# Kernel tuning notes

Measured on AMD Instinct MI355X. Metric: run time of the kernel, lower is better.

Reference implementation:

```python
import jax, jax.numpy as jnp
import numpy as np

V_TH = 1.0
LENS, SCALE, HIGHT, GAMMA = 0.5, 6.0, 0.15, 0.5  # MultiGaussian surrogate constants (DH-SNN)


def _gauss(x, mu, sigma):
    return jnp.exp(-((x - mu) ** 2) / (2.0 * sigma ** 2)) / (jnp.sqrt(2.0 * jnp.pi) * sigma)


@jax.custom_vjp
def spike_fn(x):
    return (x > 0).astype(x.dtype)


def _spike_fwd(x):
    return spike_fn(x), x


def _spike_bwd(x, g):
    sg = GAMMA * (_gauss(x, 0.0, LENS) * (1.0 + HIGHT)
                  - _gauss(x, LENS, SCALE * LENS) * HIGHT
                  - _gauss(x, -LENS, SCALE * LENS) * HIGHT)
    return (g * sg,)


spike_fn.defvjp(_spike_fwd, _spike_bwd)


def setup_inputs() -> dict:
    key = jax.random.key(0)
    ks = jax.random.split(key, 12)
    B, T, I, H, O = 128, 784, 512, 512, 10
    xavier_in = lambda k, sh: jax.random.normal(k, sh, jnp.float32) * jnp.sqrt(2.0 / (sh[0] + sh[1]))
    return {
        'input_data': jax.random.normal(ks[0], (B, T, I), jnp.float32),
        'W1': xavier_in(ks[1], (H, I)),
        'b1': jnp.zeros((H,), jnp.float32),
        'W2': xavier_in(ks[2], (H, I)),
        'b2': jnp.zeros((H,), jnp.float32),
        'tau_m': jax.random.uniform(ks[3], (H,), jnp.float32, 0.0, 4.0),
        'tau_n1': jax.random.uniform(ks[4], (H,), jnp.float32, 2.0, 6.0),
        'tau_n2': jax.random.uniform(ks[5], (H,), jnp.float32, -4.0, 0.0),
        'Wr': xavier_in(ks[6], (O, H)),
        'br': jnp.zeros((O,), jnp.float32),
        'mem0': jax.random.uniform(ks[7], (B, H), jnp.float32),
        'spike0': jax.random.uniform(ks[8], (B, H), jnp.float32),
    }


def reference(input_data, W1, b1, W2, b2, tau_m, tau_n1, tau_n2, Wr, br, mem0, spike0):
    # Batched branch projections for all timesteps (big GEMMs, done once)
    d1_all = jnp.einsum('bti,hi->bth', input_data, W1) + b1  # [B,T,H]
    d2_all = jnp.einsum('bti,hi->bth', input_data, W2) + b2

    alpha = jax.nn.sigmoid(tau_m)    # membrane decay
    beta1 = jax.nn.sigmoid(tau_n1)   # branch-1 dendritic decay
    beta2 = jax.nn.sigmoid(tau_n2)   # branch-2 dendritic decay

    B, H = mem0.shape
    d1_init = jnp.zeros((B, H), input_data.dtype)
    d2_init = jnp.zeros((B, H), input_data.dtype)

    def step(carry, xs):
        mem, spk, d1, d2 = carry
        d1_t, d2_t = xs
        d1 = beta1 * d1 + (1.0 - beta1) * d1_t
        d2 = beta2 * d2 + (1.0 - beta2) * d2_t
        total = d1 + d2
        mem = mem * alpha + (1.0 - alpha) * total - V_TH * spk
        spk = spike_fn(mem - V_TH)
        return (mem, spk, d1, d2), spk

    xs = (jnp.swapaxes(d1_all, 0, 1), jnp.swapaxes(d2_all, 0, 1))  # [T,B,H]
    _, spikes = jax.lax.scan(step, (mem0, spike0, d1_init, d2_init), xs)
    spikes = jnp.swapaxes(spikes, 0, 1)  # [B,T,H]
    out = jnp.einsum('bth,oh->bto', spikes, Wr) + br  # readout per timestep
    return out
```

## Files before the change

kernel.cpp:

```cpp
#include <hip/hip_runtime.h>
#include <cmath>

#define HD 512
#define IN 512
#define TT 784
#define BB 128
#define MH 50176

typedef short short8 __attribute__((ext_vector_type(8)));
typedef unsigned short ushort8 __attribute__((ext_vector_type(8)));
typedef float floatx4 __attribute__((ext_vector_type(4)));

#define GLDS(gp, lp) __builtin_amdgcn_global_load_lds( \
    (const __attribute__((address_space(1))) void*)(gp), \
    (__attribute__((address_space(3))) void*)(lp), 16, 0, 0)

__device__ __forceinline__ unsigned short bf16_rne(float x) {
    unsigned u = __float_as_uint(x);
    unsigned r = u + 0x7FFFu + ((u >> 16) & 1u);
    return (unsigned short)(r >> 16);
}
__device__ __forceinline__ float bf16_f(unsigned short s) {
    return __uint_as_float(((unsigned)s) << 16);
}

__global__ __launch_bounds__(256) void split3(
    const float* __restrict__ src, unsigned short* __restrict__ p1,
    unsigned short* __restrict__ p2, unsigned short* __restrict__ p3, long n8)
{
    long g = (long)blockIdx.x * 256 + threadIdx.x;
    if (g >= n8) return;
    const float* xp = src + g * 8;
    ushort8 o1, o2, o3;
#pragma unroll
    for (int j = 0; j < 8; ++j) {
        float x = xp[j];
        unsigned short s1 = bf16_rne(x);
        float r1 = x - bf16_f(s1);
        unsigned short s2 = bf16_rne(r1);
        float r2 = r1 - bf16_f(s2);
        unsigned short s3 = bf16_rne(r2);
        o1[j] = s1; o2[j] = s2; o3[j] = s3;
    }
    *(ushort8*)(p1 + g * 8) = o1;
    *(ushort8*)(p2 + g * 8) = o2;
    *(ushort8*)(p3 + g * 8) = o3;
}

__global__ __launch_bounds__(256, 2) void gemm_bf16x3(
    const unsigned short* __restrict__ Xp,
    const unsigned short* __restrict__ Wp,
    const float* __restrict__ b1, const float* __restrict__ b2,
    float* __restrict__ d1buf, float* __restrict__ d2buf)
{
    __shared__ unsigned short lds[6][128][32];
    unsigned short* lflat = &lds[0][0][0];
    const int tid  = threadIdx.x;
    const int lane = tid & 63;
    const int w    = tid >> 6;
    const int wg = (blockIdx.x & 7) * 392 + (blockIdx.x >> 3);
    const int pm = wg >> 3;
    const int pn = wg & 7;
    const int m0 = pm * 128;
    const int n0 = pn * 128;

    const unsigned short* gp[12];
    {
        const int rsub = lane >> 2;
        const int csub = (lane & 3) * 8;
#pragma unroll
        for (int j = 0; j < 12; ++j) {
            int seg = w * 12 + j;
            int p = seg >> 3, sub = seg & 7;
            int row16 = sub * 16 + rsub;
            gp[j] = (p < 3)
              ? Xp + ((size_t)p * MH + m0 + row16) * IN + csub
              : Wp + ((size_t)(p - 3) * 1024 + n0 + row16) * IN + csub;
        }
    }

    floatx4 acc[4][4];
#pragma unroll
    for (int i = 0; i < 4; ++i)
#pragma unroll
        for (int j = 0; j < 4; ++j) acc[i][j] = (floatx4){0.f, 0.f, 0.f, 0.f};

    const int wm = w >> 1, wn = w & 1;
    const int c16 = lane & 15;
    const int q8  = (lane >> 4) * 8;

    for (int ks = 0; ks < IN; ks += 32) {
#pragma unroll
        for (int j = 0; j < 12; ++j)
            GLDS(gp[j] + ks, lflat + (size_t)(w * 12 + j) * 512);
        __syncthreads();

        short8 Bf[3][4];
#pragma unroll
        for (int p = 0; p < 3; ++p)
#pragma unroll
            for (int fj = 0; fj < 4; ++fj)
                Bf[p][fj] = *(const short8*)&lds[3 + p][wn * 64 + fj * 16 + c16][q8];

#pragma unroll
        for (int fi = 0; fi < 4; ++fi) {
            const int r = wm * 64 + fi * 16 + c16;
            short8 a1 = *(const short8*)&lds[0][r][q8];
            short8 a2 = *(const short8*)&lds[1][r][q8];
            short8 a3 = *(const short8*)&lds[2][r][q8];
#pragma unroll
            for (int fj = 0; fj < 4; ++fj) {
                floatx4 c = acc[fi][fj];
                c = __builtin_amdgcn_mfma_f32_16x16x32_bf16(a3, Bf[0][fj], c, 0, 0, 0);
                c = __builtin_amdgcn_mfma_f32_16x16x32_bf16(a2, Bf[1][fj], c, 0, 0, 0);
                c = __builtin_amdgcn_mfma_f32_16x16x32_bf16(a1, Bf[2][fj], c, 0, 0, 0);
                c = __builtin_amdgcn_mfma_f32_16x16x32_bf16(a2, Bf[0][fj], c, 0, 0, 0);
                c = __builtin_amdgcn_mfma_f32_16x16x32_bf16(a1, Bf[1][fj], c, 0, 0, 0);
                c = __builtin_amdgcn_mfma_f32_16x16x32_bf16(a1, Bf[0][fj], c, 0, 0, 0);
                acc[fi][fj] = c;
            }
        }
        __syncthreads();
    }

    const int quad = lane >> 4;
    const bool first = (n0 < HD);
    const float* bias = first ? b1 : b2;
    float* obuf = first ? d1buf : d2buf;
    const int nb = n0 & (HD - 1);
    float bv[4];
#pragma unroll
    for (int fj = 0; fj < 4; ++fj) bv[fj] = bias[nb + wn * 64 + fj * 16 + c16];
#pragma unroll
    for (int fi = 0; fi < 4; ++fi) {
#pragma unroll
        for (int fj = 0; fj < 4; ++fj) {
            int n = nb + wn * 64 + fj * 16 + c16;
#pragma unroll
            for (int r = 0; r < 4; ++r) {
                int m = m0 + wm * 64 + fi * 16 + quad * 4 + r;
                obuf[(size_t)m * HD + n] = acc[fi][fj][r] + bv[fj];
            }
        }
    }
}

#define LOADG(g, A1, A2) do {                                        \
    _Pragma("unroll")                                                \
    for (int i = 0; i < 16; ++i) {                                   \
        A1[i] = p1[(size_t)((g) * 16 + i) * HD];                     \
        A2[i] = p2[(size_t)((g) * 16 + i) * HD];                     \
    } } while (0)

#define COMPG(g, A1, A2) do {                                        \
    unsigned int wq = 0;                                             \
    _Pragma("unroll")                                                \
    for (int i = 0; i < 16; ++i) {                                   \
        d1 = be1 * d1 + (1.f - be1) * A1[i];                         \
        d2 = be2 * d2 + (1.f - be2) * A2[i];                         \
        float tot = d1 + d2;                                         \
        mem = mem * alpha + (1.f - alpha) * tot - spk;               \
        bool fire = (mem - 1.0f) > 0.f;                              \
        spk = fire ? 1.f : 0.f;                                      \
        wq |= (fire ? 1u : 0u) << i;                                 \
    }                                                                \
    sp[(size_t)(g) * HD] = (unsigned short)wq; } while (0)

__global__ __launch_bounds__(64) void scan_half(
    const float* __restrict__ d1buf, const float* __restrict__ d2buf,
    const float* __restrict__ tau_m, const float* __restrict__ tau_n1,
    const float* __restrict__ tau_n2,
    const float* __restrict__ mem0, const float* __restrict__ spike0,
    unsigned short* __restrict__ spikes, int b0)
{
    const int gid = blockIdx.x * 64 + threadIdx.x;
    const int h  = gid & (HD - 1);
    const int bl = gid >> 9;
    const int b  = b0 + bl;
    const float alpha = 1.f / (1.f + expf(-tau_m[h]));
    const float be1   = 1.f / (1.f + expf(-tau_n1[h]));
    const float be2   = 1.f / (1.f + expf(-tau_n2[h]));
    float mem = mem0[b * HD + h];
    float spk = spike0[b * HD + h];
    float d1 = 0.f, d2 = 0.f;
    const float* p1 = d1buf + (size_t)bl * TT * HD + h;
    const float* p2 = d2buf + (size_t)bl * TT * HD + h;
    unsigned short* sp = spikes + (size_t)b * (TT / 16) * HD + h;

    float a1A[16], a2A[16], a1B[16], a2B[16];
    LOADG(0, a1A, a2A);
#pragma unroll 1
    for (int g = 0; g < 48; g += 2) {
        LOADG(g + 1, a1B, a2B);
        COMPG(g,     a1A, a2A);
        LOADG(g + 2, a1A, a2A);
        COMPG(g + 1, a1B, a2B);
    }
    COMPG(48, a1A, a2A);
}

__global__ __launch_bounds__(256) void readout(
    const unsigned short* __restrict__ spikes,
    const float* __restrict__ Wr, const float* __restrict__ br,
    float* __restrict__ out)
{
    __shared__ float WrS[10 * HD];
    __shared__ float brS[10];
    const int tid = threadIdx.x;
    for (int i = tid; i < 10 * HD; i += 256) WrS[i] = Wr[i];
    if (tid < 10) brS[tid] = br[tid];
    __syncthreads();

    const int gid = blockIdx.x * 256 + tid;
    const int t = gid % TT;
    const int b = gid / TT;
    const int tw  = t >> 4;
    const int bit = t & 15;
    const unsigned short* row = spikes + ((size_t)b * (TT / 16) + tw) * HD;

    float acc[10];
#pragma unroll
    for (int o = 0; o < 10; ++o) acc[o] = brS[o];

    for (int h = 0; h < HD; ++h) {
        float s = (float)((row[h] >> bit) & 1);
#pragma unroll
        for (int o = 0; o < 10; ++o) acc[o] = fmaf(s, WrS[o * HD + h], acc[o]);
    }
    float* op = out + (size_t)gid * 10;
#pragma unroll
    for (int o = 0; o < 10; ++o) op[o] = acc[o];
}

extern "C" void kernel_launch(void* const* d_in, const int* in_sizes, int n_in,
                              void* d_out, int out_size, void* d_ws, size_t ws_size,
                              hipStream_t stream)
{
    const float* X      = (const float*)d_in[0];
    const float* W1     = (const float*)d_in[1];
    const float* b1     = (const float*)d_in[2];
    const float* W2     = (const float*)d_in[3];
    const float* b2     = (const float*)d_in[4];
    const float* tau_m  = (const float*)d_in[5];
    const float* tau_n1 = (const float*)d_in[6];
    const float* tau_n2 = (const float*)d_in[7];
    const float* Wr     = (const float*)d_in[8];
    const float* br     = (const float*)d_in[9];
    const float* mem0   = (const float*)d_in[10];
    const float* spike0 = (const float*)d_in[11];
    float* out = (float*)d_out;

    char* p = (char*)d_ws;
    unsigned short* Wp = (unsigned short*)p;  p += (size_t)3 * 1024 * IN * 2;
    unsigned short* Xp = (unsigned short*)p;  p += (size_t)3 * MH * IN * 2;
    float* d1buf = (float*)p;                 p += (size_t)MH * HD * 4;
    float* d2buf = (float*)p;                 p += (size_t)MH * HD * 4;
    unsigned short* spikes = (unsigned short*)p;

    const size_t WPS = (size_t)1024 * IN;
    const size_t XPS = (size_t)MH * IN;

    split3<<<dim3(128), dim3(256), 0, stream>>>(
        W1, Wp, Wp + WPS, Wp + 2 * WPS, (long)HD * IN / 8);
    split3<<<dim3(128), dim3(256), 0, stream>>>(
        W2, Wp + (size_t)HD * IN, Wp + WPS + (size_t)HD * IN,
        Wp + 2 * WPS + (size_t)HD * IN, (long)HD * IN / 8);

    for (int half = 0; half < 2; ++half) {
        split3<<<dim3((unsigned)(((long)MH * IN / 8 + 255) / 256)), dim3(256), 0, stream>>>(
            X + (size_t)half * MH * IN, Xp, Xp + XPS, Xp + 2 * XPS, (long)MH * IN / 8);
        gemm_bf16x3<<<dim3(392 * 8), dim3(256), 0, stream>>>(
            Xp, Wp, b1, b2, d1buf, d2buf);
        scan_half<<<dim3(512), dim3(64), 0, stream>>>(
            d1buf, d2buf, tau_m, tau_n1, tau_n2, mem0, spike0,
            spikes, half * 64);
    }
    readout<<<dim3(BB * TT / 256), dim3(256), 0, stream>>>(spikes, Wr, br, out);
}
```

Measured before the change: 1.096 ms.

## Triple-buffer GEMM K loop with 32x32 MFMA and swizzled LDS layout

Rewrites the bf16x3 GEMM main loop to use a three-stage LDS ring with global_load_lds prefetch and explicit vmcnt waits, so global loads overlap with MFMA work instead of being serialized by barriers. The K step shrinks to 16 and the compute switches from 16x16x32 to 32x32x16 MFMA tiles, with an XOR-swizzled LDS layout meant to avoid bank conflicts. LDS rises to 72KB dynamic, which may limit occupancy to two blocks per CU, and the hand-written waitcnt logic is fragile.

Result: slower. 1.219 ms (+11.2%).

```diff
diff --git a/kernel.cpp b/kernel.cpp
--- a/kernel.cpp
+++ b/kernel.cpp
@@ -10,6 +10,7 @@
 typedef short short8 __attribute__((ext_vector_type(8)));
 typedef unsigned short ushort8 __attribute__((ext_vector_type(8)));
 typedef float floatx4 __attribute__((ext_vector_type(4)));
+typedef float floatx16 __attribute__((ext_vector_type(16)));
 
 #define GLDS(gp, lp) __builtin_amdgcn_global_load_lds( \
     (const __attribute__((address_space(1))) void*)(gp), \
@@ -47,14 +48,13 @@
     *(ushort8*)(p3 + g * 8) = o3;
 }
 
-__global__ __launch_bounds__(256, 2) void gemm_bf16x3(
+__global__ __launch_bounds__(256, 2) void gemm_bf16x3_p2(
     const unsigned short* __restrict__ Xp,
     const unsigned short* __restrict__ Wp,
     const float* __restrict__ b1, const float* __restrict__ b2,
     float* __restrict__ d1buf, float* __restrict__ d2buf)
 {
-    __shared__ unsigned short lds[6][128][32];
-    unsigned short* lflat = &lds[0][0][0];
+    extern __shared__ unsigned short lds[];
     const int tid  = threadIdx.x;
     const int lane = tid & 63;
     const int w    = tid >> 6;
@@ -64,82 +64,106 @@
     const int m0 = pm * 128;
     const int n0 = pn * 128;
 
-    const unsigned short* gp[12];
+    const unsigned short* gp[6];
+    unsigned loff[6];
     {
-        const int rsub = lane >> 2;
-        const int csub = (lane & 3) * 8;
-#pragma unroll
-        for (int j = 0; j < 12; ++j) {
-            int seg = w * 12 + j;
-            int p = seg >> 3, sub = seg & 7;
-            int row16 = sub * 16 + rsub;
+        const int rsub = lane >> 1;
+        const int csub = (((lane & 1) ^ ((lane >> 3) & 1)) * 8);
+#pragma unroll
+        for (int j = 0; j < 6; ++j) {
+            int s = w * 6 + j;
+            int p = s >> 2, rb = s & 3;
             gp[j] = (p < 3)
-              ? Xp + ((size_t)p * MH + m0 + row16) * IN + csub
-              : Wp + ((size_t)(p - 3) * 1024 + n0 + row16) * IN + csub;
+              ? Xp + ((size_t)p * MH + m0 + rb * 32 + rsub) * IN + csub
+              : Wp + ((size_t)(p - 3) * 1024 + n0 + rb * 32 + rsub) * IN + csub;
+            loff[j] = (unsigned)s * 512;
         }
     }
 
-    floatx4 acc[4][4];
-#pragma unroll
-    for (int i = 0; i < 4; ++i)
-#pragma unroll
-        for (int j = 0; j < 4; ++j) acc[i][j] = (floatx4){0.f, 0.f, 0.f, 0.f};
+    floatx16 acc[2][2];
+#pragma unroll
+    for (int i = 0; i < 2; ++i)
+#pragma unroll
+        for (int j = 0; j < 2; ++j)
+#pragma unroll
+            for (int r = 0; r < 16; ++r) acc[i][j][r] = 0.f;
 
     const int wm = w >> 1, wn = w & 1;
-    const int c16 = lane & 15;
-    const int q8  = (lane >> 4) * 8;
-
-    for (int ks = 0; ks < IN; ks += 32) {
-#pragma unroll
-        for (int j = 0; j < 12; ++j)
-            GLDS(gp[j] + ks, lflat + (size_t)(w * 12 + j) * 512);
-        __syncthreads();
-
-        short8 Bf[3][4];
-#pragma unroll
-        for (int p = 0; p < 3; ++p)
-#pragma unroll
-            for (int fj = 0; fj < 4; ++fj)
-                Bf[p][fj] = *(const short8*)&lds[3 + p][wn * 64 + fj * 16 + c16][q8];
-
-#pragma unroll
-        for (int fi = 0; fi < 4; ++fi) {
-            const int r = wm * 64 + fi * 16 + c16;
-            short8 a1 = *(const short8*)&lds[0][r][q8];
-            short8 a2 = *(const short8*)&lds[1][r][q8];
-            short8 a3 = *(const short8*)&lds[2][r][q8];
-#pragma unroll
-            for (int fj = 0; fj < 4; ++fj) {
-                floatx4 c = acc[fi][fj];
-                c = __builtin_amdgcn_mfma_f32_16x16x32_bf16(a3, Bf[0][fj], c, 0, 0, 0);
-                c = __builtin_amdgcn_mfma_f32_16x16x32_bf16(a2, Bf[1][fj], c, 0, 0, 0);
-                c = __builtin_amdgcn_mfma_f32_16x16x32_bf16(a1, Bf[2][fj], c, 0, 0, 0);
-                c = __builtin_amdgcn_mfma_f32_16x16x32_bf16(a2, Bf[0][fj], c, 0, 0, 0);
-                c = __builtin_amdgcn_mfma_f32_16x16x32_bf16(a1, Bf[1][fj], c, 0, 0, 0);
-                c = __builtin_amdgcn_mfma_f32_16x16x32_bf16(a1, Bf[0][fj], c, 0, 0, 0);
-                acc[fi][fj] = c;
+    const int l31 = lane & 31;
+    const int sl8 = (((lane >> 5) ^ ((lane >> 2) & 1)) & 1) * 8;
+
+    auto compute = [&](const unsigned short* buf) {
+        short8 A[2][3], B[2][3];
+#pragma unroll
+        for (int tt = 0; tt < 2; ++tt)
+#pragma unroll
+            for (int p = 0; p < 3; ++p) {
+                A[tt][p] = *(const short8*)&buf[p * 2048 +
+                    (wm * 64 + tt * 32 + l31) * 16 + sl8];
+                B[tt][p] = *(const short8*)&buf[(3 + p) * 2048 +
+                    (wn * 64 + tt * 32 + l31) * 16 + sl8];
             }
-        }
-        __syncthreads();
-    }
-
-    const int quad = lane >> 4;
+        __builtin_amdgcn_s_setprio(1);
+#pragma unroll
+        for (int ti = 0; ti < 2; ++ti)
+#pragma unroll
+            for (int tj = 0; tj < 2; ++tj) {
+                floatx16 c = acc[ti][tj];
+                c = __builtin_amdgcn_mfma_f32_32x32x16_bf16(A[ti][2], B[tj][0], c, 0, 0, 0);
+                c = __builtin_amdgcn_mfma_f32_32x32x16_bf16(A[ti][1], B[tj][1], c, 0, 0, 0);
+                c = __builtin_amdgcn_mfma_f32_32x32x16_bf16(A[ti][0], B[tj][2], c, 0, 0, 0);
+                c = __builtin_amdgcn_mfma_f32_32x32x16_bf16(A[ti][1], B[tj][0], c, 0, 0, 0);
+                c = __builtin_amdgcn_mfma_f32_32x32x16_bf16(A[ti][0], B[tj][1], c, 0, 0, 0);
+                c = __builtin_amdgcn_mfma_f32_32x32x16_bf16(A[ti][0], B[tj][0], c, 0, 0, 0);
+                acc[ti][tj] = c;
+            }
+        __builtin_amdgcn_s_setprio(0);
+    };
+
+#define STAGE(bb, t) do {                                            \
+    _Pragma("unroll")                                                \
+    for (int j = 0; j < 6; ++j)                                      \
+        GLDS(gp[j] + (t) * 16, lds + (bb) + loff[j]);                \
+    } while (0)
+
+    STAGE(0,     0);
+    STAGE(12288, 1);
+    STAGE(24576, 2);
+
+#pragma unroll 1
+    for (int t = 0; t < 32; ++t) {
+        const int b = t - (t / 3) * 3;
+        const int bb = b * 12288;
+        if (t < 30)       asm volatile("s_waitcnt vmcnt(12)" ::: "memory");
+        else if (t == 30) asm volatile("s_waitcnt vmcnt(6)"  ::: "memory");
+        else              asm volatile("s_waitcnt vmcnt(0)"  ::: "memory");
+        __builtin_amdgcn_s_barrier();
+        __builtin_amdgcn_sched_barrier(0);
+        compute(lds + bb);
+        __builtin_amdgcn_sched_barrier(0);
+        __builtin_amdgcn_s_barrier();
+        __builtin_amdgcn_sched_barrier(0);
+        if (t < 29) STAGE(bb, t + 3);
+    }
+#undef STAGE
+
+    const int rhi = (lane >> 5) * 4;
     const bool first = (n0 < HD);
     const float* bias = first ? b1 : b2;
     float* obuf = first ? d1buf : d2buf;
     const int nb = n0 & (HD - 1);
-    float bv[4];
-#pragma unroll
-    for (int fj = 0; fj < 4; ++fj) bv[fj] = bias[nb + wn * 64 + fj * 16 + c16];
-#pragma unroll
-    for (int fi = 0; fi < 4; ++fi) {
-#pragma unroll
-        for (int fj = 0; fj < 4; ++fj) {
-            int n = nb + wn * 64 + fj * 16 + c16;
-#pragma unroll
-            for (int r = 0; r < 4; ++r) {
-                int m = m0 + wm * 64 + fi * 16 + quad * 4 + r;
-                obuf[(size_t)m * HD + n] = acc[fi][fj][r] + bv[fj];
+    float bv[2];
+#pragma unroll
+    for (int tj = 0; tj < 2; ++tj) bv[tj] = bias[nb + wn * 64 + tj * 32 + l31];
+#pragma unroll
+    for (int ti = 0; ti < 2; ++ti) {
+#pragma unroll
+        for (int tj = 0; tj < 2; ++tj) {
+            int n = nb + wn * 64 + tj * 32 + l31;
+#pragma unroll
+            for (int r = 0; r < 16; ++r) {
+                int m = m0 + wm * 64 + ti * 32 + (r & 3) + 8 * (r >> 2) + rhi;
+                obuf[(size_t)m * HD + n] = acc[ti][tj][r] + bv[tj];
             }
         }
     }
@@ -250,6 +274,14 @@
     const float* spike0 = (const float*)d_in[11];
     float* out = (float*)d_out;
 
+    static int s_attr = 0;
+    if (!s_attr) {
+        (void)hipFuncSetAttribute(
+            reinterpret_cast<const void*>(gemm_bf16x3_p2),
+            hipFuncAttributeMaxDynamicSharedMemorySize, 73728);
+        s_attr = 1;
+    }
+
     char* p = (char*)d_ws;
     unsigned short* Wp = (unsigned short*)p;  p += (size_t)3 * 1024 * IN * 2;
     unsigned short* Xp = (unsigned short*)p;  p += (size_t)3 * MH * IN * 2;
@@ -269,7 +301,7 @@
     for (int half = 0; half < 2; ++half) {
         split3<<<dim3((unsigned)(((long)MH * IN / 8 + 255) / 256)), dim3(256), 0, stream>>>(
             X + (size_t)half * MH * IN, Xp, Xp + XPS, Xp + 2 * XPS, (long)MH * IN / 8);
-        gemm_bf16x3<<<dim3(392 * 8), dim3(256), 0, stream>>>(
+        gemm_bf16x3_p2<<<dim3(392 * 8), dim3(256), 73728, stream>>>(
             Xp, Wp, b1, b2, d1buf, d2buf);
         scan_half<<<dim3(512), dim3(64), 0, stream>>>(
             d1buf, d2buf, tau_m, tau_n1, tau_n2, mem0, spike0,
```

## Fuse fp32-to-bf16x3 split of input into GEMM A-tile loading

Applied to the files above, without the earlier changes.

Removes the separate split3 pass over the large input activation tensor. The GEMM now loads fp32 X directly into registers, splits it into three bf16 parts with packed convert instructions, and writes them to LDS. The loop is software-pipelined: register prefetch of the next A tile overlaps the current compute, with explicit waitcnt and barriers. This saves a full write and re-read of the tripled bf16 copy of X, but each GEMM block now re-splits its A tile once per N-tile (8 times across the grid) and reads fp32 data, which doubles the bytes per element loaded.

Measured after the change: 937.8 us. -14.5%, faster.

```diff
diff --git a/kernel.cpp b/kernel.cpp
--- a/kernel.cpp
+++ b/kernel.cpp
@@ -10,10 +10,13 @@
 typedef short short8 __attribute__((ext_vector_type(8)));
 typedef unsigned short ushort8 __attribute__((ext_vector_type(8)));
 typedef float floatx4 __attribute__((ext_vector_type(4)));
+typedef unsigned int uintx4 __attribute__((ext_vector_type(4)));
 
 #define GLDS(gp, lp) __builtin_amdgcn_global_load_lds( \
     (const __attribute__((address_space(1))) void*)(gp), \
     (__attribute__((address_space(3))) void*)(lp), 16, 0, 0)
+
+#define CVTPK(d, a, b) asm("v_cvt_pk_bf16_f32 %0, %1, %2" : "=v"(d) : "v"(a), "v"(b))
 
 __device__ __forceinline__ unsigned short bf16_rne(float x) {
     unsigned u = __float_as_uint(x);
@@ -47,8 +50,8 @@
     *(ushort8*)(p3 + g * 8) = o3;
 }
 
-__global__ __launch_bounds__(256, 2) void gemm_bf16x3(
-    const unsigned short* __restrict__ Xp,
+__global__ __launch_bounds__(256, 2) void gemm_fused(
+    const float* __restrict__ Xf,
     const unsigned short* __restrict__ Wp,
     const float* __restrict__ b1, const float* __restrict__ b2,
     float* __restrict__ d1buf, float* __restrict__ d2buf)
@@ -64,20 +67,24 @@
     const int m0 = pm * 128;
     const int n0 = pn * 128;
 
-    const unsigned short* gp[12];
+    const unsigned short* gpb[6];
+    unsigned lofb[6];
     {
         const int rsub = lane >> 2;
         const int csub = (lane & 3) * 8;
 #pragma unroll
-        for (int j = 0; j < 12; ++j) {
-            int seg = w * 12 + j;
-            int p = seg >> 3, sub = seg & 7;
-            int row16 = sub * 16 + rsub;
-            gp[j] = (p < 3)
-              ? Xp + ((size_t)p * MH + m0 + row16) * IN + csub
-              : Wp + ((size_t)(p - 3) * 1024 + n0 + row16) * IN + csub;
+        for (int j = 0; j < 6; ++j) {
+            int s = w * 6 + j;
+            int p = s >> 3, sub = s & 7;
+            gpb[j] = Wp + ((size_t)p * 1024 + n0 + sub * 16 + rsub) * IN + csub;
+            lofb[j] = 12288u + (unsigned)s * 512;
         }
     }
+
+    const int arow  = tid >> 1;
+    const int ahalf = tid & 1;
+    const float* ga = Xf + (size_t)(m0 + arow) * IN + ahalf * 16;
+    const int awbase = arow * 32 + ahalf * 16;
 
     floatx4 acc[4][4];
 #pragma unroll
@@ -89,39 +96,94 @@
     const int c16 = lane & 15;
     const int q8  = (lane >> 4) * 8;
 
-    for (int ks = 0; ks < IN; ks += 32) {
-#pragma unroll
-        for (int j = 0; j < 12; ++j)
-            GLDS(gp[j] + ks, lflat + (size_t)(w * 12 + j) * 512);
-        __syncthreads();
-
-        short8 Bf[3][4];
-#pragma unroll
-        for (int p = 0; p < 3; ++p)
-#pragma unroll
-            for (int fj = 0; fj < 4; ++fj)
-                Bf[p][fj] = *(const short8*)&lds[3 + p][wn * 64 + fj * 16 + c16][q8];
-
-#pragma unroll
-        for (int fi = 0; fi < 4; ++fi) {
-            const int r = wm * 64 + fi * 16 + c16;
-            short8 a1 = *(const short8*)&lds[0][r][q8];
-            short8 a2 = *(const short8*)&lds[1][r][q8];
-            short8 a3 = *(const short8*)&lds[2][r][q8];
-#pragma unroll
-            for (int fj = 0; fj < 4; ++fj) {
-                floatx4 c = acc[fi][fj];
-                c = __builtin_amdgcn_mfma_f32_16x16x32_bf16(a3, Bf[0][fj], c, 0, 0, 0);
-                c = __builtin_amdgcn_mfma_f32_16x16x32_bf16(a2, Bf[1][fj], c, 0, 0, 0);
-                c = __builtin_amdgcn_mfma_f32_16x16x32_bf16(a1, Bf[2][fj], c, 0, 0, 0);
-                c = __builtin_amdgcn_mfma_f32_16x16x32_bf16(a2, Bf[0][fj], c, 0, 0, 0);
-                c = __builtin_amdgcn_mfma_f32_16x16x32_bf16(a1, Bf[1][fj], c, 0, 0, 0);
-                c = __builtin_amdgcn_mfma_f32_16x16x32_bf16(a1, Bf[0][fj], c, 0, 0, 0);
-                acc[fi][fj] = c;
-            }
-        }
-        __syncthreads();
-    }
+#define LOADA(DST, T) do {                                           \
+    _Pragma("unroll")                                                \
+    for (int q = 0; q < 4; ++q)                                      \
+        DST[q] = *(const floatx4*)(ga + (T) * 32 + q * 4);           \
+    } while (0)
+
+#define SPLITW(SRC) do {                                             \
+    unsigned w1[8], w2[8], w3[8];                                    \
+    _Pragma("unroll")                                                \
+    for (int q = 0; q < 4; ++q) {                                    \
+        _Pragma("unroll")                                            \
+        for (int e = 0; e < 2; ++e) {                                \
+            float x0 = SRC[q][e * 2], x1 = SRC[q][e * 2 + 1];        \
+            unsigned pk1, pk2, pk3;                                  \
+            CVTPK(pk1, x0, x1);                                      \
+            float r0 = x0 - __uint_as_float(pk1 << 16);              \
+            float r1 = x1 - __uint_as_float(pk1 & 0xFFFF0000u);      \
+            CVTPK(pk2, r0, r1);                                      \
+            float s0 = r0 - __uint_as_float(pk2 << 16);              \
+            float s1 = r1 - __uint_as_float(pk2 & 0xFFFF0000u);      \
+            CVTPK(pk3, s0, s1);                                      \
+            w1[q * 2 + e] = pk1; w2[q * 2 + e] = pk2; w3[q * 2 + e] = pk3; \
+        }                                                            \
+    }                                                                \
+    *(uintx4*)(lflat + awbase)            = (uintx4){w1[0], w1[1], w1[2], w1[3]}; \
+    *(uintx4*)(lflat + awbase + 8)        = (uintx4){w1[4], w1[5], w1[6], w1[7]}; \
+    *(uintx4*)(lflat + 4096 + awbase)     = (uintx4){w2[0], w2[1], w2[2], w2[3]}; \
+    *(uintx4*)(lflat + 4096 + awbase + 8) = (uintx4){w2[4], w2[5], w2[6], w2[7]}; \
+    *(uintx4*)(lflat + 8192 + awbase)     = (uintx4){w3[0], w3[1], w3[2], w3[3]}; \
+    *(uintx4*)(lflat + 8192 + awbase + 8) = (uintx4){w3[4], w3[5], w3[6], w3[7]}; \
+    } while (0)
+
+#define COMPUTE() do {                                               \
+    short8 Bf[3][4];                                                 \
+    _Pragma("unroll")                                                \
+    for (int p = 0; p < 3; ++p)                                      \
+        _Pragma("unroll")                                            \
+        for (int fj = 0; fj < 4; ++fj)                               \
+            Bf[p][fj] = *(const short8*)&lds[3 + p][wn * 64 + fj * 16 + c16][q8]; \
+    _Pragma("unroll")                                                \
+    for (int fi = 0; fi < 4; ++fi) {                                 \
+        const int r = wm * 64 + fi * 16 + c16;                       \
+        short8 a1 = *(const short8*)&lds[0][r][q8];                  \
+        short8 a2 = *(const short8*)&lds[1][r][q8];                  \
+        short8 a3 = *(const short8*)&lds[2][r][q8];                  \
+        _Pragma("unroll")                                            \
+        for (int fj = 0; fj < 4; ++fj) {                             \
+            floatx4 c = acc[fi][fj];                                 \
+            c = __builtin_amdgcn_mfma_f32_16x16x32_bf16(a3, Bf[0][fj], c, 0, 0, 0); \
+            c = __builtin_amdgcn_mfma_f32_16x16x32_bf16(a2, Bf[1][fj], c, 0, 0, 0); \
+            c = __builtin_amdgcn_mfma_f32_16x16x32_bf16(a1, Bf[2][fj], c, 0, 0, 0); \
+            c = __builtin_amdgcn_mfma_f32_16x16x32_bf16(a2, Bf[0][fj], c, 0, 0, 0); \
+            c = __builtin_amdgcn_mfma_f32_16x16x32_bf16(a1, Bf[1][fj], c, 0, 0, 0); \
+            c = __builtin_amdgcn_mfma_f32_16x16x32_bf16(a1, Bf[0][fj], c, 0, 0, 0); \
+            acc[fi][fj] = c;                                         \
+        }                                                            \
+    } } while (0)
+
+#define BAR() asm volatile("s_barrier" ::: "memory")
+
+    floatx4 xa[4], xb[4];
+    LOADA(xa, 0);
+
+#pragma unroll 1
+    for (int tp = 0; tp < 8; ++tp) {
+        const int t0 = tp * 2, t1 = tp * 2 + 1;
+#pragma unroll
+        for (int j = 0; j < 6; ++j) GLDS(gpb[j] + t0 * 32, lflat + lofb[j]);
+        LOADA(xb, t1);
+        SPLITW(xa);
+        asm volatile("s_waitcnt vmcnt(4) lgkmcnt(0)" ::: "memory");
+        BAR();
+        COMPUTE();
+        BAR();
+#pragma unroll
+        for (int j = 0; j < 6; ++j) GLDS(gpb[j] + t1 * 32, lflat + lofb[j]);
+        if (tp < 7) LOADA(xa, t1 + 1);
+        SPLITW(xb);
+        if (tp < 7) asm volatile("s_waitcnt vmcnt(4) lgkmcnt(0)" ::: "memory");
+        else        asm volatile("s_waitcnt vmcnt(0) lgkmcnt(0)" ::: "memory");
+        BAR();
+        COMPUTE();
+        BAR();
+    }
+#undef LOADA
+#undef SPLITW
+#undef COMPUTE
+#undef BAR
 
     const int quad = lane >> 4;
     const bool first = (n0 < HD);
@@ -252,13 +314,11 @@
 
     char* p = (char*)d_ws;
     unsigned short* Wp = (unsigned short*)p;  p += (size_t)3 * 1024 * IN * 2;
-    unsigned short* Xp = (unsigned short*)p;  p += (size_t)3 * MH * IN * 2;
     float* d1buf = (float*)p;                 p += (size_t)MH * HD * 4;
     float* d2buf = (float*)p;                 p += (size_t)MH * HD * 4;
     unsigned short* spikes = (unsigned short*)p;
 
     const size_t WPS = (size_t)1024 * IN;
-    const size_t XPS = (size_t)MH * IN;
 
     split3<<<dim3(128), dim3(256), 0, stream>>>(
         W1, Wp, Wp + WPS, Wp + 2 * WPS, (long)HD * IN / 8);
@@ -267,10 +327,8 @@
         Wp + 2 * WPS + (size_t)HD * IN, (long)HD * IN / 8);
 
     for (int half = 0; half < 2; ++half) {
-        split3<<<dim3((unsigned)(((long)MH * IN / 8 + 255) / 256)), dim3(256), 0, stream>>>(
-            X + (size_t)half * MH * IN, Xp, Xp + XPS, Xp + 2 * XPS, (long)MH * IN / 8);
-        gemm_bf16x3<<<dim3(392 * 8), dim3(256), 0, stream>>>(
-            Xp, Wp, b1, b2, d1buf, d2buf);
+        gemm_fused<<<dim3(392 * 8), dim3(256), 0, stream>>>(
+            X + (size_t)half * MH * IN, Wp, b1, b2, d1buf, d2buf);
         scan_half<<<dim3(512), dim3(64), 0, stream>>>(
             d1buf, d2buf, tau_m, tau_n1, tau_n2, mem0, spike0,
             spikes, half * 64);
```
